# Kernel optimization log

Measured on AMD Instinct MI355X. Metric: run time of the kernel, lower is better.

Reference implementation:

```python
import jax, jax.numpy as jnp
import numpy as np
import math

D_MODEL = 2048
NUM_HEADS = 16
D_HEAD = D_MODEL // NUM_HEADS
MAX_SEQ_LEN = 2048
THETA = 10000.0
B, T = 2, 2048


def setup_inputs() -> dict:
    key = jax.random.key(0)
    ks = jax.random.split(key, 5)
    s = 1.0 / math.sqrt(D_MODEL)
    return {
        "x": jax.random.normal(ks[0], (B, T, D_MODEL), dtype=jnp.float32),
        "token_positions": jnp.arange(T, dtype=jnp.int64 if jax.config.jax_enable_x64 else jnp.int32),
        "Wq": jax.random.normal(ks[1], (D_MODEL, D_MODEL), dtype=jnp.float32) * s,
        "Wk": jax.random.normal(ks[2], (D_MODEL, D_MODEL), dtype=jnp.float32) * s,
        "Wv": jax.random.normal(ks[3], (D_MODEL, D_MODEL), dtype=jnp.float32) * s,
        "Wproj": jax.random.normal(ks[4], (D_MODEL, D_MODEL), dtype=jnp.float32) * s,
    }


def _rope_tables(dtype):
    inv_freq = 1.0 / (THETA ** (jnp.arange(0, D_HEAD, 2, dtype=jnp.float32) / D_HEAD))
    angle = jnp.arange(MAX_SEQ_LEN, dtype=jnp.float32)[:, None] * inv_freq[None, :]  # [S, d/2]
    return jnp.cos(angle).astype(dtype), jnp.sin(angle).astype(dtype)


def _apply_rope(x, cos, sin):
    # x: [B, H, T, d_head]; cos/sin: [T, d_head/2] (broadcast over B,H)
    x1 = x[..., 0::2]
    x2 = x[..., 1::2]
    o1 = x1 * cos - x2 * sin
    o2 = x1 * sin + x2 * cos
    return jnp.stack([o1, o2], axis=-1).reshape(x.shape)


def reference(x, token_positions, Wq, Wk, Wv, Wproj):
    Bx, Tx, D = x.shape
    # Linear layers: weight [out, in], no bias
    q = (x @ Wq.T).reshape(Bx, Tx, NUM_HEADS, D_HEAD).transpose(0, 2, 1, 3)
    k = (x @ Wk.T).reshape(Bx, Tx, NUM_HEADS, D_HEAD).transpose(0, 2, 1, 3)
    v = (x @ Wv.T).reshape(Bx, Tx, NUM_HEADS, D_HEAD).transpose(0, 2, 1, 3)

    cos_t, sin_t = _rope_tables(x.dtype)
    cos = cos_t[token_positions]  # [T, d_head/2]
    sin = sin_t[token_positions]
    q = _apply_rope(q, cos, sin)
    k = _apply_rope(k, cos, sin)

    scale = 1.0 / math.sqrt(D_HEAD)
    scores = jnp.einsum("bhqd,bhkd->bhqk", q, k) * scale
    causal = jnp.tril(jnp.ones((Tx, Tx), dtype=bool))
    scores = jnp.where(causal, scores, -jnp.inf)
    attn = jax.nn.softmax(scores, axis=-1)
    o = jnp.einsum("bhqk,bhkd->bhqd", attn, v)  # [B, H, T, d_head]
    o = o.transpose(0, 2, 1, 3).reshape(Bx, Tx, D)
    return o @ Wproj.T
```

## Files before the change

kernel.cpp:

```cpp
#include <hip/hip_runtime.h>
#include <hip/hip_bf16.h>

#define DM    2048
#define NH    16
#define DHD   128
#define TSEQ  2048
#define NBB   2
#define NTOK  (NBB*TSEQ)

typedef __attribute__((ext_vector_type(8))) short bf16x8;
typedef __attribute__((ext_vector_type(4))) float f32x4;

typedef __attribute__((address_space(1))) const void GVoid;
typedef __attribute__((address_space(3))) void LVoid;
#define GLOAD16(SRC, DST) __builtin_amdgcn_global_load_lds((GVoid*)(SRC), (LVoid*)(DST), 16, 0, 0)

__device__ __forceinline__ unsigned short f2bf(float f) {
  union { float f; unsigned u; } v; v.f = f;
  unsigned r = v.u + 0x7fffu + ((v.u >> 16) & 1u);
  return (unsigned short)(r >> 16);
}
__device__ __forceinline__ float bf2f(unsigned short h) {
  union { unsigned u; float f; } v; v.u = ((unsigned)h) << 16;
  return v.f;
}

#define QSCALE (0.08838834764831845f * 1.4426950408889634f)

__global__ void cvt_kernel(const float* __restrict__ in, unsigned short* __restrict__ out, int n4) {
  int i = blockIdx.x * blockDim.x + threadIdx.x;
  int stride = gridDim.x * blockDim.x;
  for (; i < n4; i += stride) {
    float4 v = reinterpret_cast<const float4*>(in)[i];
    ushort4 o;
    o.x = f2bf(v.x); o.y = f2bf(v.y); o.z = f2bf(v.z); o.w = f2bf(v.w);
    reinterpret_cast<ushort4*>(out)[i] = o;
  }
}

__global__ void cvt4_kernel(const float* __restrict__ a, const float* __restrict__ b,
                           const float* __restrict__ c, const float* __restrict__ d,
                           unsigned short* __restrict__ out, int n4per) {
  const float* in = (blockIdx.y == 0) ? a : (blockIdx.y == 1) ? b : (blockIdx.y == 2) ? c : d;
  unsigned short* o = out + (size_t)blockIdx.y * (size_t)n4per * 4;
  int i = blockIdx.x * blockDim.x + threadIdx.x;
  int stride = gridDim.x * blockDim.x;
  for (; i < n4per; i += stride) {
    float4 v = reinterpret_cast<const float4*>(in)[i];
    ushort4 ov;
    ov.x = f2bf(v.x); ov.y = f2bf(v.y); ov.z = f2bf(v.z); ov.w = f2bf(v.w);
    reinterpret_cast<ushort4*>(o)[i] = ov;
  }
}

__global__ void rope_table_kernel(const int* __restrict__ pos, float* __restrict__ ctab, float* __restrict__ stab) {
  int idx = blockIdx.x * blockDim.x + threadIdx.x;
  if (idx >= TSEQ * 64) return;
  int i = idx & 63;
  int t = idx >> 6;
  float freq = expf(-(2.0f * i / 128.0f) * 9.210340371976184f);
  float ang = (float)pos[t] * freq;
  ctab[idx] = cosf(ang);
  stab[idx] = sinf(ang);
}

#define G2M 256
#define G2N 128
#define G2K 64
template<int MODE>
__global__ __launch_bounds__(512, 2) void gemm256(
    const unsigned short* __restrict__ A,
    const unsigned short* __restrict__ Bt,
    void* __restrict__ Cp,
    unsigned short* __restrict__ QrO, unsigned short* __restrict__ KrO,
    const float* __restrict__ ct, const float* __restrict__ st,
    int K, int N, int NBN) {
  __shared__ unsigned short lds[3 * (G2M + G2N) * G2K];
  const int t = threadIdx.x;
  const int lane = t & 63, w = t >> 6;
  const int wr = w >> 2, wc = w & 3;
  const int lr = lane & 15, lg = lane >> 4;
  const int nwg = gridDim.x;
  const int swz = (blockIdx.x & 7) * (nwg >> 3) + (blockIdx.x >> 3);
  const int m0 = (swz / NBN) * G2M;
  const int n0g = (swz % NBN) * G2N;
  const int NT = K / G2K;

  f32x4 acc[8][2] = {};

  auto stageA = [&](int kt, int b) {
    unsigned short* dst = &lds[b * (G2M + G2N) * G2K];
    const size_t k0 = (size_t)kt * G2K;
    #pragma unroll
    for (int c = 0; c < 4; c++) {
      int i = c * 512 + t;
      int row = i >> 3, slot = i & 7;
      int sslot = slot ^ (row & 7);
      GLOAD16(A + (size_t)(m0 + row) * K + k0 + sslot * 8,
              dst + (size_t)(c * 512 + w * 64) * 8);
    }
  };
  auto stageB = [&](int kt, int b) {
    unsigned short* dst = &lds[b * (G2M + G2N) * G2K + G2M * G2K];
    const size_t k0 = (size_t)kt * G2K;
    #pragma unroll
    for (int c = 0; c < 2; c++) {
      int i = c * 512 + t;
      int row = i >> 3, slot = i & 7;
      int sslot = slot ^ (row & 7);
      GLOAD16(Bt + (size_t)(n0g + row) * K + k0 + sslot * 8,
              dst + (size_t)(c * 512 + w * 64) * 8);
    }
  };

  const unsigned short* bufA = nullptr;
  const unsigned short* bufB = nullptr;
  auto ldA = [&](int mi, int ks) -> bf16x8 {
    int r = wr * 128 + mi * 16 + lr;
    int cb = (ks * 64 + lg * 16) ^ ((r & 7) << 4);
    return *(const bf16x8*)((const char*)bufA + r * 128 + cb);
  };
  auto ldB = [&](int ni, int ks) -> bf16x8 {
    int r = wc * 32 + ni * 16 + lr;
    int cb = (ks * 64 + lg * 16) ^ ((r & 7) << 4);
    return *(const bf16x8*)((const char*)bufB + r * 128 + cb);
  };

  stageA(0, 0); stageB(0, 0);
  stageA(1, 1); stageB(1, 1);

  for (int kt = 0; kt < NT; kt++) {
    if (kt + 1 < NT) { asm volatile("s_waitcnt vmcnt(6)" ::: "memory"); }
    else             { asm volatile("s_waitcnt vmcnt(0)" ::: "memory"); }
    __builtin_amdgcn_s_barrier();
    const int b = kt % 3;
    bufA = &lds[b * (G2M + G2N) * G2K];
    bufB = bufA + G2M * G2K;
    const int kt2 = kt + 2, b2 = kt2 % 3;

    bf16x8 bfr[2][2], afr[4][2];
    #pragma unroll
    for (int ni = 0; ni < 2; ni++)
      #pragma unroll
      for (int ks = 0; ks < 2; ks++) bfr[ni][ks] = ldB(ni, ks);
    #pragma unroll
    for (int mi = 0; mi < 4; mi++)
      #pragma unroll
      for (int ks = 0; ks < 2; ks++) afr[mi][ks] = ldA(mi, ks);
    if (kt2 < NT) stageA(kt2, b2);
    asm volatile("s_waitcnt lgkmcnt(0)" ::: "memory");
    __builtin_amdgcn_sched_barrier(0);
    __builtin_amdgcn_s_setprio(1);
    #pragma unroll
    for (int mi = 0; mi < 4; mi++)
      #pragma unroll
      for (int ni = 0; ni < 2; ni++)
        #pragma unroll
        for (int ks = 0; ks < 2; ks++)
          acc[mi][ni] = __builtin_amdgcn_mfma_f32_16x16x32_bf16(afr[mi][ks], bfr[ni][ks], acc[mi][ni], 0, 0, 0);
    __builtin_amdgcn_s_setprio(0);
    __builtin_amdgcn_s_barrier();

    bf16x8 afr2[4][2];
    #pragma unroll
    for (int mi = 0; mi < 4; mi++)
      #pragma unroll
      for (int ks = 0; ks < 2; ks++) afr2[mi][ks] = ldA(mi + 4, ks);
    if (kt2 < NT) stageB(kt2, b2);
    asm volatile("s_waitcnt lgkmcnt(0)" ::: "memory");
    __builtin_amdgcn_sched_barrier(0);
    __builtin_amdgcn_s_setprio(1);
    #pragma unroll
    for (int mi = 0; mi < 4; mi++)
      #pragma unroll
      for (int ni = 0; ni < 2; ni++)
        #pragma unroll
        for (int ks = 0; ks < 2; ks++)
          acc[mi + 4][ni] = __builtin_amdgcn_mfma_f32_16x16x32_bf16(afr2[mi][ks], bfr[ni][ks], acc[mi + 4][ni], 0, 0, 0);
    __builtin_amdgcn_s_setprio(0);
  }

  if (MODE == 0) {
    #pragma unroll
    for (int mi = 0; mi < 8; mi++)
      #pragma unroll
      for (int j = 0; j < 4; j++) {
        int row = m0 + wr * 128 + mi * 16 + lg * 4 + j;
        #pragma unroll
        for (int ni = 0; ni < 2; ni++) {
          int cg = n0g + wc * 32 + ni * 16 + lr;
          ((float*)Cp)[(size_t)row * N + cg] = acc[mi][ni][j];
        }
      }
  } else {
    const int sel = n0g >> 11;
    if (sel == 2) {
      __builtin_amdgcn_s_barrier();
      unsigned short* Lt = lds;
      #pragma unroll
      for (int mi = 0; mi < 8; mi++)
        #pragma unroll
        for (int j = 0; j < 4; j++) {
          int tl = wr * 128 + mi * 16 + lg * 4 + j;
          #pragma unroll
          for (int ni = 0; ni < 2; ni++) {
            int d = wc * 32 + ni * 16 + lr;
            Lt[d * 264 + tl] = f2bf(acc[mi][ni][j]);
          }
        }
      __builtin_amdgcn_s_barrier();
      const int hh = (n0g & 2047) >> 7;
      const int bb = m0 >> 11, t0 = m0 & (TSEQ - 1);
      const int bh = bb * NH + hh;
      unsigned short* VtO = (unsigned short*)Cp;
      #pragma unroll
      for (int c = 0; c < 8; c++) {
        int ci = c * 512 + t;
        int d = ci >> 5, tc = ci & 31;
        bf16x8 v = *(const bf16x8*)&Lt[d * 264 + tc * 8];
        *(bf16x8*)&VtO[((size_t)bh * DHD + d) * TSEQ + t0 + tc * 8] = v;
      }
    } else {
      unsigned short* dst = sel ? KrO : QrO;
      const float qm = sel ? 1.0f : QSCALE;
      #pragma unroll
      for (int mi = 0; mi < 8; mi++)
        #pragma unroll
        for (int j = 0; j < 4; j++) {
          int row = m0 + wr * 128 + mi * 16 + lg * 4 + j;
          int bb = row >> 11, tt = row & (TSEQ - 1);
          #pragma unroll
          for (int ni = 0; ni < 2; ni++) {
            int c2 = (n0g + wc * 32 + ni * 16 + lr) & 2047;
            int d = c2 & 127, hh = c2 >> 7;
            float v = acc[mi][ni][j];
            float px = __shfl_xor(v, 1);
            float cc = ct[tt * 64 + (d >> 1)], ss = st[tt * 64 + (d >> 1)];
            float o = (d & 1) ? (px * ss + v * cc) : (v * cc - px * ss);
            dst[(((size_t)(bb * NH + hh)) * TSEQ + tt) * DHD + d] = f2bf(o * qm);
          }
        }
    }
  }
}

__global__ __launch_bounds__(512, 4) void attn_kernel(
    const unsigned short* __restrict__ Qr,
    const unsigned short* __restrict__ Kr,
    const unsigned short* __restrict__ VTt,
    unsigned short* __restrict__ Oa) {
  __shared__ unsigned short Ks[64 * 128];
  __shared__ unsigned short Vs[128 * 64];
  __shared__ unsigned short Ps[8 * 16 * 64];
  const int t = threadIdx.x;
  const int lane = t & 63, w = t >> 6;
  const int wv = w & 3, half = w >> 2;
  const int lr = lane & 15, lg = lane >> 4;
  const int p = blockIdx.x, bh = blockIdx.y;
  const int qA = p, qB = 31 - p;
  const int myq = half ? qA : qB;
  const int q0 = myq * 64;
  const int nt = myq + 1;
  const int ntB = qB + 1;
  const unsigned short* Qh = Qr + (size_t)bh * TSEQ * DHD;
  const unsigned short* Kh = Kr + (size_t)bh * TSEQ * DHD;
  const unsigned short* Vh = VTt + (size_t)bh * DHD * TSEQ;

  bf16x8 qf[4];
  #pragma unroll
  for (int ks = 0; ks < 4; ks++)
    qf[ks] = *(const bf16x8*)&Qh[((size_t)(q0 + wv * 16 + lr)) * DHD + ks * 32 + lg * 8];

  f32x4 oacc[8] = {};
  float ps[4] = {};
  unsigned short* Pw = &Ps[w * 16 * 64];

  for (int jt = 0; jt < ntB; jt++) {
    const int j0 = jt * 64;
    #pragma unroll
    for (int c = 0; c < 2; c++) {
      int ci = c * 512 + t;
      int row = ci >> 4, slot = ci & 15;
      GLOAD16(Kh + (size_t)(j0 + row) * DHD + (slot ^ (row & 7)) * 8,
              &Ks[(c * 512 + w * 64) * 8]);
    }
    #pragma unroll
    for (int c = 0; c < 2; c++) {
      int ci = c * 512 + t;
      int row = ci >> 3, slot = ci & 7;
      GLOAD16(Vh + (size_t)row * TSEQ + j0 + (slot ^ (row & 7)) * 8,
              &Vs[(c * 512 + w * 64) * 8]);
    }
    __syncthreads();
    if (jt < nt) {
      const bool diag = (jt == nt - 1);
      f32x4 sv[4] = {};
      #pragma unroll
      for (int n = 0; n < 4; n++) {
        #pragma unroll
        for (int ks = 0; ks < 4; ks++) {
          int row = n * 16 + lr;
          int byteoff = row * 256 + (((ks * 64 + lg * 16)) ^ ((row & 7) << 4));
          bf16x8 kf = *(const bf16x8*)((const char*)Ks + byteoff);
          sv[n] = __builtin_amdgcn_mfma_f32_16x16x32_bf16(qf[ks], kf, sv[n], 0, 0, 0);
        }
      }
      if (diag) {
        #pragma unroll
        for (int n = 0; n < 4; n++) {
          int kcol = j0 + n * 16 + lr;
          #pragma unroll
          for (int j = 0; j < 4; j++)
            if (kcol > q0 + wv * 16 + lg * 4 + j) sv[n][j] = -INFINITY;
        }
      }
      #pragma unroll
      for (int n = 0; n < 4; n++) {
        #pragma unroll
        for (int j = 0; j < 4; j++) {
          float pv = exp2f(sv[n][j]);
          ps[j] += pv;
          int prow = lg * 4 + j;
          int pcol = n * 16 + lr;
          int byteoff = (prow * 128 + pcol * 2) ^ ((prow & 7) << 4);
          *(unsigned short*)((char*)Pw + byteoff) = f2bf(pv);
        }
      }
      bf16x8 pa[2];
      #pragma unroll
      for (int kk = 0; kk < 2; kk++) {
        int byteoff = lr * 128 + (((kk * 64 + lg * 16)) ^ ((lr & 7) << 4));
        pa[kk] = *(const bf16x8*)((const char*)Pw + byteoff);
      }
      #pragma unroll
      for (int n2 = 0; n2 < 8; n2++) {
        #pragma unroll
        for (int kk = 0; kk < 2; kk++) {
          int row = n2 * 16 + lr;
          int byteoff = row * 128 + (((kk * 64 + lg * 16)) ^ ((row & 7) << 4));
          bf16x8 vf = *(const bf16x8*)((const char*)Vs + byteoff);
          oacc[n2] = __builtin_amdgcn_mfma_f32_16x16x32_bf16(pa[kk], vf, oacc[n2], 0, 0, 0);
        }
      }
    }
    __syncthreads();
  }

  #pragma unroll
  for (int m = 1; m < 16; m <<= 1)
    #pragma unroll
    for (int j = 0; j < 4; j++) ps[j] += __shfl_xor(ps[j], m);
  const int h = bh & (NH - 1), b = bh >> 4;
  #pragma unroll
  for (int j = 0; j < 4; j++) {
    float inv = 1.0f / ps[j];
    int tt = q0 + wv * 16 + lg * 4 + j;
    size_t base = ((size_t)(b * TSEQ + tt)) * DM + h * DHD;
    #pragma unroll
    for (int n2 = 0; n2 < 8; n2++)
      Oa[base + n2 * 16 + lr] = f2bf(oacc[n2][j] * inv);
  }
}

extern "C" void kernel_launch(void* const* d_in, const int* in_sizes, int n_in,
                              void* d_out, int out_size, void* d_ws, size_t ws_size,
                              hipStream_t stream) {
  const float* x  = (const float*)d_in[0];
  const int*   pos = (const int*)d_in[1];
  const float* Wq = (const float*)d_in[2];
  const float* Wk = (const float*)d_in[3];
  const float* Wv = (const float*)d_in[4];
  const float* Wp = (const float*)d_in[5];
  float* out = (float*)d_out;

  char* wsp = (char*)d_ws;
  auto alloc = [&](size_t bytes) { char* p = wsp; wsp += (bytes + 255) & ~(size_t)255; return p; };
  unsigned short* xb  = (unsigned short*)alloc((size_t)NTOK * DM * 2);
  unsigned short* wqb = (unsigned short*)alloc((size_t)DM * DM * 2);
  unsigned short* wkb = (unsigned short*)alloc((size_t)DM * DM * 2);
  unsigned short* wvb = (unsigned short*)alloc((size_t)DM * DM * 2);
  unsigned short* wpb = (unsigned short*)alloc((size_t)DM * DM * 2);
  unsigned short* Qb  = (unsigned short*)alloc((size_t)NTOK * DM * 2);
  unsigned short* Kb  = (unsigned short*)alloc((size_t)NTOK * DM * 2);
  unsigned short* VTt = (unsigned short*)alloc((size_t)NTOK * DM * 2);
  float* ctab = (float*)alloc((size_t)TSEQ * 64 * 4);
  float* stab = (float*)alloc((size_t)TSEQ * 64 * 4);
  unsigned short* Oa = xb;
  (void)wkb; (void)wvb;

  int n4x = NTOK * DM / 4, n4w = DM * DM / 4;
  cvt_kernel<<<2048, 256, 0, stream>>>(x, xb, n4x);
  cvt4_kernel<<<dim3(256, 4), 256, 0, stream>>>(Wq, Wk, Wv, Wp, wqb, n4w);
  rope_table_kernel<<<(TSEQ * 64) / 256, 256, 0, stream>>>(pos, ctab, stab);

  gemm256<1><<<(NTOK / G2M) * (3 * DM / G2N), 512, 0, stream>>>(
      xb, wqb, VTt, Qb, Kb, ctab, stab, DM, DM, 3 * DM / G2N);

  attn_kernel<<<dim3(16, NBB * NH), 512, 0, stream>>>(Qb, Kb, VTt, Oa);

  gemm256<0><<<(NTOK / G2M) * (DM / G2N), 512, 0, stream>>>(
      Oa, wpb, out, nullptr, nullptr, nullptr, nullptr, DM, DM, DM / G2N);
}
```

Measured before the change: 241.0 us.

## Split fused QKV GEMM into square-tile Q/K GEMM with RoPE and separate V GEMM

Replaces the single 256x128-tile GEMM producing Q, K and transposed V with two launches. The first is a new 256x256-tile, K-step-32, 4-buffer GEMM that computes Q and K with fused RoPE and the Q scale. The second is the existing gemm256 in a V-only transpose mode. Larger square tiles raise arithmetic intensity and cut redundant A-tile loads for Q/K, and branch divergence in the epilogue is removed. The cost is an extra kernel launch, higher register pressure from 32 accumulators per thread, and a smaller K step per barrier.

Measured after the change: 238.9 us. About the same (-0.9%).

```diff
diff --git a/kernel.cpp b/kernel.cpp
--- a/kernel.cpp
+++ b/kernel.cpp
@@ -64,6 +64,126 @@
   stab[idx] = sinf(ang);
 }
 
+#define QM  256
+#define QN  256
+#define QKS 32
+#define QLDSB ((QM + QN) * QKS)
+__global__ __launch_bounds__(512, 2) void gemmsq(
+    const unsigned short* __restrict__ A,
+    const unsigned short* __restrict__ Bt,
+    unsigned short* __restrict__ QrO, unsigned short* __restrict__ KrO,
+    const float* __restrict__ ct, const float* __restrict__ st,
+    int K, int NBN) {
+  __shared__ unsigned short lds[4 * QLDSB];
+  const int t = threadIdx.x;
+  const int lane = t & 63, w = t >> 6;
+  const int wr = w >> 2, wc = w & 3;
+  const int lr = lane & 15, lg = lane >> 4;
+  const int nwg = gridDim.x;
+  const int swz = (blockIdx.x & 7) * (nwg >> 3) + (blockIdx.x >> 3);
+  const int m0 = (swz / NBN) * QM;
+  const int n0g = (swz % NBN) * QN;
+  const int NT = K / QKS;
+
+  f32x4 acc[8][4] = {};
+
+  auto stageA = [&](int kt, int b) {
+    unsigned short* dst = &lds[b * QLDSB];
+    const size_t k0 = (size_t)kt * QKS;
+    #pragma unroll
+    for (int c = 0; c < 2; c++) {
+      int ci = c * 512 + t;
+      int row = ci >> 2, slot = ci & 3;
+      GLOAD16(A + (size_t)(m0 + row) * K + k0 + slot * 8,
+              dst + (size_t)(c * 512 + w * 64) * 8);
+    }
+  };
+  auto stageB = [&](int kt, int b) {
+    unsigned short* dst = &lds[b * QLDSB + QM * QKS];
+    const size_t k0 = (size_t)kt * QKS;
+    #pragma unroll
+    for (int c = 0; c < 2; c++) {
+      int ci = c * 512 + t;
+      int row = ci >> 2, slot = ci & 3;
+      GLOAD16(Bt + (size_t)(n0g + row) * K + k0 + slot * 8,
+              dst + (size_t)(c * 512 + w * 64) * 8);
+    }
+  };
+
+  const unsigned short* buf = nullptr;
+  auto ldA = [&](int mi) -> bf16x8 {
+    int r = wr * 128 + mi * 16 + lr;
+    return *(const bf16x8*)((const char*)buf + r * 64 + lg * 16);
+  };
+  auto ldB = [&](int ni) -> bf16x8 {
+    int r = wc * 64 + ni * 16 + lr;
+    return *(const bf16x8*)((const char*)(buf + QM * QKS) + r * 64 + lg * 16);
+  };
+
+  stageA(0, 0); stageB(0, 0);
+  stageA(1, 1); stageB(1, 1);
+
+  for (int kt = 0; kt < NT; kt++) {
+    if (kt + 1 < NT) { asm volatile("s_waitcnt vmcnt(4)" ::: "memory"); }
+    else             { asm volatile("s_waitcnt vmcnt(0)" ::: "memory"); }
+    __builtin_amdgcn_s_barrier();
+    buf = &lds[(kt & 3) * QLDSB];
+    const int kt2 = kt + 2, b2 = kt2 & 3;
+
+    bf16x8 bfr[4], afr[4];
+    #pragma unroll
+    for (int ni = 0; ni < 4; ni++) bfr[ni] = ldB(ni);
+    #pragma unroll
+    for (int mi = 0; mi < 4; mi++) afr[mi] = ldA(mi);
+    if (kt2 < NT) stageA(kt2, b2);
+    asm volatile("s_waitcnt lgkmcnt(0)" ::: "memory");
+    __builtin_amdgcn_sched_barrier(0);
+    __builtin_amdgcn_s_setprio(1);
+    #pragma unroll
+    for (int mi = 0; mi < 4; mi++)
+      #pragma unroll
+      for (int ni = 0; ni < 4; ni++)
+        acc[mi][ni] = __builtin_amdgcn_mfma_f32_16x16x32_bf16(afr[mi], bfr[ni], acc[mi][ni], 0, 0, 0);
+    __builtin_amdgcn_s_setprio(0);
+    __builtin_amdgcn_s_barrier();
+
+    bf16x8 afr2[4];
+    #pragma unroll
+    for (int mi = 0; mi < 4; mi++) afr2[mi] = ldA(mi + 4);
+    if (kt2 < NT) stageB(kt2, b2);
+    asm volatile("s_waitcnt lgkmcnt(0)" ::: "memory");
+    __builtin_amdgcn_sched_barrier(0);
+    __builtin_amdgcn_s_setprio(1);
+    #pragma unroll
+    for (int mi = 0; mi < 4; mi++)
+      #pragma unroll
+      for (int ni = 0; ni < 4; ni++)
+        acc[mi + 4][ni] = __builtin_amdgcn_mfma_f32_16x16x32_bf16(afr2[mi], bfr[ni], acc[mi + 4][ni], 0, 0, 0);
+    __builtin_amdgcn_s_setprio(0);
+  }
+
+  const int selK = n0g >> 11;
+  unsigned short* dst = selK ? KrO : QrO;
+  const float qm = selK ? 1.0f : QSCALE;
+  #pragma unroll
+  for (int mi = 0; mi < 8; mi++)
+    #pragma unroll
+    for (int j = 0; j < 4; j++) {
+      int row = m0 + wr * 128 + mi * 16 + lg * 4 + j;
+      int bb = row >> 11, tt = row & (TSEQ - 1);
+      #pragma unroll
+      for (int ni = 0; ni < 4; ni++) {
+        int c2 = (n0g + wc * 64 + ni * 16 + lr) & 2047;
+        int d = c2 & 127, hh = c2 >> 7;
+        float v = acc[mi][ni][j];
+        float px = __shfl_xor(v, 1);
+        float cc = ct[tt * 64 + (d >> 1)], ss = st[tt * 64 + (d >> 1)];
+        float o = (d & 1) ? (px * ss + v * cc) : (v * cc - px * ss);
+        dst[(((size_t)(bb * NH + hh)) * TSEQ + tt) * DHD + d] = f2bf(o * qm);
+      }
+    }
+}
+
 #define G2M 256
 #define G2N 128
 #define G2K 64
@@ -71,10 +191,7 @@
 __global__ __launch_bounds__(512, 2) void gemm256(
     const unsigned short* __restrict__ A,
     const unsigned short* __restrict__ Bt,
-    void* __restrict__ Cp,
-    unsigned short* __restrict__ QrO, unsigned short* __restrict__ KrO,
-    const float* __restrict__ ct, const float* __restrict__ st,
-    int K, int N, int NBN) {
+    void* __restrict__ Cp, int K, int N, int NBN) {
   __shared__ unsigned short lds[3 * (G2M + G2N) * G2K];
   const int t = threadIdx.x;
   const int lane = t & 63, w = t >> 6;
@@ -193,53 +310,30 @@
         }
       }
   } else {
-    const int sel = n0g >> 11;
-    if (sel == 2) {
-      __builtin_amdgcn_s_barrier();
-      unsigned short* Lt = lds;
-      #pragma unroll
-      for (int mi = 0; mi < 8; mi++)
-        #pragma unroll
-        for (int j = 0; j < 4; j++) {
-          int tl = wr * 128 + mi * 16 + lg * 4 + j;
-          #pragma unroll
-          for (int ni = 0; ni < 2; ni++) {
-            int d = wc * 32 + ni * 16 + lr;
-            Lt[d * 264 + tl] = f2bf(acc[mi][ni][j]);
-          }
+    __builtin_amdgcn_s_barrier();
+    unsigned short* Lt = lds;
+    #pragma unroll
+    for (int mi = 0; mi < 8; mi++)
+      #pragma unroll
+      for (int j = 0; j < 4; j++) {
+        int tl = wr * 128 + mi * 16 + lg * 4 + j;
+        #pragma unroll
+        for (int ni = 0; ni < 2; ni++) {
+          int d = wc * 32 + ni * 16 + lr;
+          Lt[d * 264 + tl] = f2bf(acc[mi][ni][j]);
         }
-      __builtin_amdgcn_s_barrier();
-      const int hh = (n0g & 2047) >> 7;
-      const int bb = m0 >> 11, t0 = m0 & (TSEQ - 1);
-      const int bh = bb * NH + hh;
-      unsigned short* VtO = (unsigned short*)Cp;
-      #pragma unroll
-      for (int c = 0; c < 8; c++) {
-        int ci = c * 512 + t;
-        int d = ci >> 5, tc = ci & 31;
-        bf16x8 v = *(const bf16x8*)&Lt[d * 264 + tc * 8];
-        *(bf16x8*)&VtO[((size_t)bh * DHD + d) * TSEQ + t0 + tc * 8] = v;
-      }
-    } else {
-      unsigned short* dst = sel ? KrO : QrO;
-      const float qm = sel ? 1.0f : QSCALE;
-      #pragma unroll
-      for (int mi = 0; mi < 8; mi++)
-        #pragma unroll
-        for (int j = 0; j < 4; j++) {
-          int row = m0 + wr * 128 + mi * 16 + lg * 4 + j;
-          int bb = row >> 11, tt = row & (TSEQ - 1);
-          #pragma unroll
-          for (int ni = 0; ni < 2; ni++) {
-            int c2 = (n0g + wc * 32 + ni * 16 + lr) & 2047;
-            int d = c2 & 127, hh = c2 >> 7;
-            float v = acc[mi][ni][j];
-            float px = __shfl_xor(v, 1);
-            float cc = ct[tt * 64 + (d >> 1)], ss = st[tt * 64 + (d >> 1)];
-            float o = (d & 1) ? (px * ss + v * cc) : (v * cc - px * ss);
-            dst[(((size_t)(bb * NH + hh)) * TSEQ + tt) * DHD + d] = f2bf(o * qm);
-          }
-        }
+      }
+    __builtin_amdgcn_s_barrier();
+    const int hh = n0g >> 7;
+    const int bb = m0 >> 11, t0 = m0 & (TSEQ - 1);
+    const int bh = bb * NH + hh;
+    unsigned short* VtO = (unsigned short*)Cp;
+    #pragma unroll
+    for (int c = 0; c < 8; c++) {
+      int ci = c * 512 + t;
+      int d = ci >> 5, tc = ci & 31;
+      bf16x8 v = *(const bf16x8*)&Lt[d * 264 + tc * 8];
+      *(bf16x8*)&VtO[((size_t)bh * DHD + d) * TSEQ + t0 + tc * 8] = v;
     }
   }
 }
@@ -386,18 +480,21 @@
   float* ctab = (float*)alloc((size_t)TSEQ * 64 * 4);
   float* stab = (float*)alloc((size_t)TSEQ * 64 * 4);
   unsigned short* Oa = xb;
-  (void)wkb; (void)wvb;
+  (void)wkb;
 
   int n4x = NTOK * DM / 4, n4w = DM * DM / 4;
   cvt_kernel<<<2048, 256, 0, stream>>>(x, xb, n4x);
   cvt4_kernel<<<dim3(256, 4), 256, 0, stream>>>(Wq, Wk, Wv, Wp, wqb, n4w);
   rope_table_kernel<<<(TSEQ * 64) / 256, 256, 0, stream>>>(pos, ctab, stab);
 
-  gemm256<1><<<(NTOK / G2M) * (3 * DM / G2N), 512, 0, stream>>>(
-      xb, wqb, VTt, Qb, Kb, ctab, stab, DM, DM, 3 * DM / G2N);
+  gemmsq<<<(NTOK / QM) * (2 * DM / QN), 512, 0, stream>>>(
+      xb, wqb, Qb, Kb, ctab, stab, DM, 2 * DM / QN);
+
+  gemm256<2><<<(NTOK / G2M) * (DM / G2N), 512, 0, stream>>>(
+      xb, wvb, VTt, DM, DM, DM / G2N);
 
   attn_kernel<<<dim3(16, NBB * NH), 512, 0, stream>>>(Qb, Kb, VTt, Oa);
 
   gemm256<0><<<(NTOK / G2M) * (DM / G2N), 512, 0, stream>>>(
-      Oa, wpb, out, nullptr, nullptr, nullptr, nullptr, DM, DM, DM / G2N);
-}
+      Oa, wpb, out, DM, DM, DM / G2N);
+}
```
